# Kernel tuning notes

Measured on AMD Instinct MI355X. Metric: run time of the kernel, lower is better.

## Reference

```python
import jax, jax.numpy as jnp
import numpy as np

N = 50000      # nodes
E = 800000     # edges
IN = 128       # in_channels
HID = 64       # hidden_channels (per head)
HEADS = 2      # GAT heads
OUT = 64       # out_channels (classes)


def segment_softmax(e, seg, num_segments):
    # softmax of per-edge scores grouped by destination node
    m = jax.ops.segment_max(e, seg, num_segments=num_segments)
    ex = jnp.exp(e - m[seg])
    s = jax.ops.segment_sum(ex, seg, num_segments=num_segments)
    return ex / s[seg]


def setup_inputs() -> dict:
    key = jax.random.key(0)
    ks = jax.random.split(key, 12)
    sc = 0.05
    return {
        "x": jax.random.normal(ks[0], (N, IN), dtype=jnp.float32),
        "edge_index": jax.random.randint(ks[1], (2, E), 0, N),
        # GATConv params: lin (no bias), att_src/att_dst, output bias
        "W1": jax.random.normal(ks[2], (IN, HEADS * HID), dtype=jnp.float32) * sc,
        "att_src": jax.random.normal(ks[3], (HEADS, HID), dtype=jnp.float32) * sc,
        "att_dst": jax.random.normal(ks[4], (HEADS, HID), dtype=jnp.float32) * sc,
        "b1": jnp.zeros((HEADS * HID,), dtype=jnp.float32),
        # TransformerConv params (heads=1): q/k/v linears + skip linear
        "Wq": jax.random.normal(ks[5], (HEADS * HID, OUT), dtype=jnp.float32) * sc,
        "bq": jnp.zeros((OUT,), dtype=jnp.float32),
        "Wk": jax.random.normal(ks[6], (HEADS * HID, OUT), dtype=jnp.float32) * sc,
        "bk": jnp.zeros((OUT,), dtype=jnp.float32),
        "Wv": jax.random.normal(ks[7], (HEADS * HID, OUT), dtype=jnp.float32) * sc,
        "bv": jnp.zeros((OUT,), dtype=jnp.float32),
        "Wskip": jax.random.normal(ks[8], (HEADS * HID, OUT), dtype=jnp.float32) * sc,
        "bskip": jnp.zeros((OUT,), dtype=jnp.float32),
    }


def reference(x, edge_index, W1, att_src, att_dst, b1,
              Wq, bq, Wk, bk, Wv, bv, Wskip, bskip):
    n = x.shape[0]
    # ---- GATConv (concat=True, add_self_loops=True, negative_slope=0.2) ----
    loops = jnp.arange(n)
    src = jnp.concatenate([edge_index[0], loops])  # message source j
    dst = jnp.concatenate([edge_index[1], loops])  # message target i
    h = (x @ W1).reshape(n, HEADS, HID)            # [N,H,C]
    a_src = (h * att_src).sum(-1)                  # [N,H]
    a_dst = (h * att_dst).sum(-1)                  # [N,H]
    e = jax.nn.leaky_relu(a_src[src] + a_dst[dst], 0.2)   # [E+N,H]
    alpha = segment_softmax(e, dst, n)                     # [E+N,H]
    out1 = jax.ops.segment_sum(alpha[..., None] * h[src], dst, num_segments=n)
    x1 = jax.nn.relu(out1.reshape(n, HEADS * HID) + b1)    # [N,H*C]
    # ---- TransformerConv (heads=1, root_weight=True, no self-loops) ----
    q = x1 @ Wq + bq
    k = x1 @ Wk + bk
    v = x1 @ Wv + bv
    s2, d2 = edge_index[0], edge_index[1]
    scores = (q[d2] * k[s2]).sum(-1) / jnp.sqrt(jnp.float32(OUT))  # [E]
    al = segment_softmax(scores, d2, n)
    agg = jax.ops.segment_sum(al[:, None] * v[s2], d2, num_segments=n)
    out = agg + x1 @ Wskip + bskip
    return jax.nn.log_softmax(out, axis=1)
```

## Files before the change

kernel.cpp:

```cpp
#include <hip/hip_runtime.h>
#include <math.h>

typedef unsigned short u16;
typedef unsigned int u32;
typedef unsigned char u8;

using bf16x8 = __attribute__((ext_vector_type(8))) short;
using f32x4  = __attribute__((ext_vector_type(4))) float;
typedef __attribute__((ext_vector_type(2))) float vf2;

#define CAP 4096

__device__ __forceinline__ float lrelu02(float x){ return x > 0.f ? x : 0.2f * x; }

__device__ __forceinline__ float bf2f(u16 u){
  union { u32 i; float f; } v; v.i = ((u32)u) << 16; return v.f;
}
__device__ __forceinline__ u16 f2bf(float f){
  union { float ff; u32 i; } v; v.ff = f;
  u32 x = v.i;
  return (u16)((x + 0x7fffu + ((x >> 16) & 1u)) >> 16);
}
__device__ __forceinline__ u32 pack2(float lo, float hi){
  return (u32)f2bf(lo) | ((u32)f2bf(hi) << 16);
}
__device__ __forceinline__ u8 f2fp8(float v){
  return (u8)(__builtin_amdgcn_cvt_pk_fp8_f32(v, v, 0, false) & 0xff);
}
__device__ __forceinline__ vf2 fma2(vf2 a, vf2 b, vf2 c){
  return __builtin_elementwise_fma(a, b, c);
}

__global__ __launch_bounds__(256) void prep_w_kernel(const float* __restrict__ W1,
                                                     const float* __restrict__ Wq,
                                                     const float* __restrict__ Wk,
                                                     const float* __restrict__ Wv,
                                                     const float* __restrict__ Ws,
                                                     const float* __restrict__ att_src,
                                                     const float* __restrict__ att_dst,
                                                     u16* __restrict__ w1t,
                                                     u16* __restrict__ wt2,
                                                     u16* __restrict__ wxt,
                                                     int* __restrict__ bcur){
  int idx = blockIdx.x * 256 + threadIdx.x;
  if (idx < 16384){
    int j = idx >> 7, k = idx & 127;
    w1t[j * 128 + k] = f2bf(W1[k * 128 + j]);
  } else if (idx < 49152){
    int i = idx - 16384;
    int mat = i >> 13;
    int r = i & 8191;
    int j = r >> 7, k = r & 127;
    const float* W = (mat == 0) ? Wq : (mat == 1) ? Wk : (mat == 2) ? Wv : Ws;
    wt2[(mat * 64 + j) * 128 + k] = f2bf(W[k * 64 + j]);
  } else if (idx < 49664){
    int i = idx - 49152;
    int j = i >> 7, k = i & 127;
    const float* av = (j & 2) ? att_dst : att_src;
    int head = j & 1;
    float s = 0.f;
#pragma unroll 8
    for (int c = 0; c < 64; c++) s += W1[k * 128 + head * 64 + c] * av[head * 64 + c];
    wxt[j * 128 + k] = f2bf(s);
  } else if (idx < 51200){
    int i = idx - 49664;
    wxt[512 + i] = 0;
  } else if (idx < 51712){
    int b = idx - 51200;
    bcur[b] = b * CAP;
  }
}

__global__ __launch_bounds__(256) void gemm1_mfma(const float* __restrict__ x,
                                                  const u16* __restrict__ w1t,
                                                  const u16* __restrict__ wxt,
                                                  u8* __restrict__ h8,
                                                  float* __restrict__ asrc,
                                                  float* __restrict__ adst, int n){
  __shared__ u8 lds8[64 * 128];
  int wid = threadIdx.x >> 6, lane = threadIdx.x & 63;
  int rl = lane & 15, kh = lane >> 4;
  int br = blockIdx.x * 64 + wid * 16;
  int arow = br + rl; if (arow > n - 1) arow = n - 1;
  const float* ab = x + (size_t)arow * 128 + kh * 8;
  f32x4 acc[9];
#pragma unroll
  for (int t = 0; t < 9; t++) acc[t] = (f32x4){0.f, 0.f, 0.f, 0.f};
#pragma unroll
  for (int ks = 0; ks < 4; ks++){
    float4 xa = *(const float4*)(ab + ks * 32);
    float4 xb = *(const float4*)(ab + ks * 32 + 4);
    union { bf16x8 v; u32 w[4]; } au;
    au.w[0] = pack2(xa.x, xa.y);
    au.w[1] = pack2(xa.z, xa.w);
    au.w[2] = pack2(xb.x, xb.y);
    au.w[3] = pack2(xb.z, xb.w);
    bf16x8 a = au.v;
#pragma unroll
    for (int t = 0; t < 8; t++){
      bf16x8 b = *(const bf16x8*)(w1t + (size_t)(t * 16 + rl) * 128 + ks * 32 + kh * 8);
      acc[t] = __builtin_amdgcn_mfma_f32_16x16x32_bf16(a, b, acc[t], 0, 0, 0);
    }
    bf16x8 bx = *(const bf16x8*)(wxt + (size_t)rl * 128 + ks * 32 + kh * 8);
    acc[8] = __builtin_amdgcn_mfma_f32_16x16x32_bf16(a, bx, acc[8], 0, 0, 0);
  }
#pragma unroll
  for (int r = 0; r < 4; r++){
    int rloc = wid * 16 + kh * 4 + r;
#pragma unroll
    for (int t = 0; t < 8; t++)
      lds8[rloc * 128 + t * 16 + rl] = f2fp8(acc[t][r]);
    int orow = br + kh * 4 + r;
    if (orow < n && rl < 4){
      float vlv = acc[8][r];
      if (rl < 2) asrc[orow * 2 + rl] = vlv;
      else        adst[orow * 2 + (rl - 2)] = vlv;
    }
  }
  int rrow = wid * 16 + (lane >> 2);
  int cb = (lane & 3) * 32;
  int grow = blockIdx.x * 64 + rrow;
  if (grow < n){
    uint4 v0 = *(const uint4*)&lds8[rrow * 128 + cb];
    uint4 v1 = *(const uint4*)&lds8[rrow * 128 + cb + 16];
    uint4* gp = (uint4*)(h8 + (size_t)grow * 128 + cb);
    gp[0] = v0;
    gp[1] = v1;
  }
}

__global__ __launch_bounds__(256) void gemm2_mfma(const u16* __restrict__ x1bf,
                                                  const u16* __restrict__ wt2,
                                                  const float* __restrict__ bq,
                                                  const float* __restrict__ bk,
                                                  const float* __restrict__ bv,
                                                  const float* __restrict__ bs,
                                                  float* __restrict__ q,
                                                  u8* __restrict__ kv8,
                                                  float* __restrict__ skip, int n){
  int wid = threadIdx.x >> 6, lane = threadIdx.x & 63;
  int rl = lane & 15, kh = lane >> 4;
  int br = blockIdx.x * 64 + wid * 16;
  int arow = br + rl; if (arow > n - 1) arow = n - 1;
  const u16* abase = x1bf + (size_t)arow * 128 + kh * 8;
  f32x4 acc[16];
#pragma unroll
  for (int t = 0; t < 16; t++) acc[t] = (f32x4){0.f, 0.f, 0.f, 0.f};
#pragma unroll
  for (int ks = 0; ks < 4; ks++){
    bf16x8 a = *(const bf16x8*)(abase + ks * 32);
#pragma unroll
    for (int t = 0; t < 16; t++){
      bf16x8 b = *(const bf16x8*)(wt2 + (size_t)(t * 16 + rl) * 128 + ks * 32 + kh * 8);
      acc[t] = __builtin_amdgcn_mfma_f32_16x16x32_bf16(a, b, acc[t], 0, 0, 0);
    }
  }
  float bias_t[16];
#pragma unroll
  for (int t = 0; t < 16; t++){
    const float* bb = (t < 4) ? bq : (t < 8) ? bk : (t < 12) ? bv : bs;
    bias_t[t] = bb[(t & 3) * 16 + rl];
  }
  int orow0 = br + kh * 4;
#pragma unroll
  for (int r = 0; r < 4; r++){
    int orow = orow0 + r;
    if (orow >= n) continue;
#pragma unroll
    for (int t = 0; t < 16; t++){
      int c = (t & 3) * 16 + rl;
      float val = acc[t][r] + bias_t[t];
      if (t < 4)       q[(size_t)orow * 64 + c]    = val;
      else if (t < 8)  kv8[(size_t)orow * 128 + (c >> 3) * 16 + (c & 7)]     = f2fp8(val);
      else if (t < 12) kv8[(size_t)orow * 128 + (c >> 3) * 16 + 8 + (c & 7)] = f2fp8(val);
      else             skip[(size_t)orow * 64 + c] = val;
    }
  }
}

__global__ __launch_bounds__(256) void multisplit_kernel(const int* __restrict__ src,
                                                         const int* __restrict__ dst,
                                                         int* __restrict__ bcur,
                                                         uint2* __restrict__ ebuf, int E){
  __shared__ int h[512];
  __shared__ int gb[512];
  __shared__ int cur[512];
  int tid = threadIdx.x;
  for (int i = tid; i < 512; i += 256){ h[i] = 0; cur[i] = 0; }
  __syncthreads();
  int base = blockIdx.x * 4096;
  int myd[16];
#pragma unroll
  for (int i = 0; i < 16; i++){
    int e = base + i * 256 + tid;
    myd[i] = (e < E) ? dst[e] : -1;
    if (myd[i] >= 0) atomicAdd(&h[myd[i] >> 7], 1);
  }
  __syncthreads();
  for (int i = tid; i < 512; i += 256){
    int c = h[i];
    gb[i] = c ? atomicAdd(&bcur[i], c) : 0;
  }
  __syncthreads();
#pragma unroll
  for (int i = 0; i < 16; i++){
    if (myd[i] >= 0){
      int e = base + i * 256 + tid;
      int b = myd[i] >> 7;
      int r = atomicAdd(&cur[b], 1);
      uint2 ed; ed.x = (u32)src[e]; ed.y = (u32)myd[i];
      ebuf[gb[b] + r] = ed;
    }
  }
}

__global__ __launch_bounds__(256) void bucket_csr_kernel(const uint2* __restrict__ ebuf,
                                                         const int* __restrict__ bcur,
                                                         const float* __restrict__ asrc,
                                                         const float* __restrict__ adst,
                                                         uint2* __restrict__ offs,
                                                         uint2* __restrict__ cpe,
                                                         int n){
  __shared__ int deg[128];
  __shared__ int loff[128];
  __shared__ int cur[128];
  int b = blockIdx.x, tid = threadIdx.x;
  int base = b * CAP, end = bcur[b];
  if (tid < 128) deg[tid] = 0;
  __syncthreads();
  for (int e = base + tid; e < end; e += 256)
    atomicAdd(&deg[ebuf[e].y & 127], 1);
  __syncthreads();
  if (tid < 64){
    int v0 = deg[2 * tid], v1 = deg[2 * tid + 1];
    int s = v0 + v1, incl = s;
#pragma unroll
    for (int o = 1; o < 64; o <<= 1){
      int t = __shfl_up(incl, o);
      if (tid >= o) incl += t;
    }
    int excl = incl - s;
    loff[2 * tid] = excl; loff[2 * tid + 1] = excl + v0;
  }
  __syncthreads();
  int node0 = b << 7;
  if (tid < 128){
    cur[tid] = loff[tid];
    int node = node0 + tid;
    if (node < n){
      uint2 ov;
      ov.x = (u32)(base + loff[tid]);
      ov.y = (u32)(base + loff[tid] + deg[tid]);
      offs[node] = ov;
    }
  }
  __syncthreads();
  for (int e = base + tid; e < end; e += 256){
    uint2 ed = ebuf[e];
    int li = (int)(ed.y & 127);
    int r = atomicAdd(&cur[li], 1);
    int sj = (int)ed.x;
    float2 as = ((const float2*)asrc)[sj];
    float2 ad = ((const float2*)adst)[node0 + li];
    uint2 cv;
    cv.x = (u32)sj;
    cv.y = pack2(__expf(lrelu02(as.x + ad.x)),
                 __expf(lrelu02(as.y + ad.y)));
    cpe[base + r] = cv;
  }
}

__global__ __launch_bounds__(256) void gat_agg_kernel(const u8* __restrict__ h8,
                                                      const float* __restrict__ asrc,
                                                      const float* __restrict__ adst,
                                                      const uint2* __restrict__ offs,
                                                      const uint2* __restrict__ cpe,
                                                      const float* __restrict__ b1,
                                                      u16* __restrict__ x1bf, int n){
  int node = blockIdx.x * 4 + (threadIdx.x >> 6);
  int lane = threadIdx.x & 63;
  if (node >= n) return;
  uint2 ov = offs[node];
  int s0 = (int)ov.x;
  int d  = (int)(ov.y - ov.x);
  int g = lane >> 3;
  int sub = lane & 7;
  int chb = sub * 16;
  int head = sub >> 2;
  float2 ad  = ((const float2*)adst)[node];
  float2 asl = ((const float2*)asrc)[node];
  float ad_own = head ? ad.y : ad.x;
  float pself = __expf(lrelu02((head ? asl.y : asl.x) + ad_own));
  vf2 acc[8];
#pragma unroll
  for (int i = 0; i < 8; i++) acc[i] = (vf2){0.f, 0.f};
  float ps = 0.f;
#pragma unroll 2
  for (int base = 0; base < d; base += 8){
    int idx = base + g;
    bool valid = idx < d;
    int ee = s0 + (valid ? idx : d - 1);
    uint2 ce = cpe[ee];
    int sj = (int)ce.x;
    float p = valid ? bf2f((u16)(head ? (ce.y >> 16) : (ce.y & 0xffffu))) : 0.f;
    ps += p;
    uint4 w = *(const uint4*)(h8 + (size_t)sj * 128 + chb);
    vf2 p2 = {p, p};
    acc[0] = fma2(p2, __builtin_amdgcn_cvt_pk_f32_fp8((int)w.x, false), acc[0]);
    acc[1] = fma2(p2, __builtin_amdgcn_cvt_pk_f32_fp8((int)w.x, true),  acc[1]);
    acc[2] = fma2(p2, __builtin_amdgcn_cvt_pk_f32_fp8((int)w.y, false), acc[2]);
    acc[3] = fma2(p2, __builtin_amdgcn_cvt_pk_f32_fp8((int)w.y, true),  acc[3]);
    acc[4] = fma2(p2, __builtin_amdgcn_cvt_pk_f32_fp8((int)w.z, false), acc[4]);
    acc[5] = fma2(p2, __builtin_amdgcn_cvt_pk_f32_fp8((int)w.z, true),  acc[5]);
    acc[6] = fma2(p2, __builtin_amdgcn_cvt_pk_f32_fp8((int)w.w, false), acc[6]);
    acc[7] = fma2(p2, __builtin_amdgcn_cvt_pk_f32_fp8((int)w.w, true),  acc[7]);
  }
#pragma unroll
  for (int o = 8; o <= 32; o <<= 1){
#pragma unroll
    for (int i = 0; i < 8; i++){
      acc[i][0] += __shfl_xor(acc[i][0], o);
      acc[i][1] += __shfl_xor(acc[i][1], o);
    }
    ps += __shfl_xor(ps, o);
  }
  if (lane < 8){
    float st = ps + pself;
    uint4 w = *(const uint4*)(h8 + (size_t)node * 128 + chb);
    vf2 pf2 = {pself, pself};
    acc[0] = fma2(pf2, __builtin_amdgcn_cvt_pk_f32_fp8((int)w.x, false), acc[0]);
    acc[1] = fma2(pf2, __builtin_amdgcn_cvt_pk_f32_fp8((int)w.x, true),  acc[1]);
    acc[2] = fma2(pf2, __builtin_amdgcn_cvt_pk_f32_fp8((int)w.y, false), acc[2]);
    acc[3] = fma2(pf2, __builtin_amdgcn_cvt_pk_f32_fp8((int)w.y, true),  acc[3]);
    acc[4] = fma2(pf2, __builtin_amdgcn_cvt_pk_f32_fp8((int)w.z, false), acc[4]);
    acc[5] = fma2(pf2, __builtin_amdgcn_cvt_pk_f32_fp8((int)w.z, true),  acc[5]);
    acc[6] = fma2(pf2, __builtin_amdgcn_cvt_pk_f32_fp8((int)w.w, false), acc[6]);
    acc[7] = fma2(pf2, __builtin_amdgcn_cvt_pk_f32_fp8((int)w.w, true),  acc[7]);
    const float4* bp = (const float4*)(b1 + chb);
    float4 bv0 = bp[0], bv1 = bp[1], bv2 = bp[2], bv3 = bp[3];
    float bb[16] = {bv0.x, bv0.y, bv0.z, bv0.w, bv1.x, bv1.y, bv1.z, bv1.w,
                    bv2.x, bv2.y, bv2.z, bv2.w, bv3.x, bv3.y, bv3.z, bv3.w};
    float inv = 1.f / st;
    u32 wv[8];
#pragma unroll
    for (int i = 0; i < 8; i++){
      float v0 = fmaxf(acc[i][0] * inv + bb[2*i],   0.f);
      float v1 = fmaxf(acc[i][1] * inv + bb[2*i+1], 0.f);
      wv[i] = pack2(v0, v1);
    }
    uint4 o0 = {wv[0], wv[1], wv[2], wv[3]};
    uint4 o1 = {wv[4], wv[5], wv[6], wv[7]};
    u16* xp = x1bf + (size_t)node * 128 + chb;
    *(uint4*)xp = o0;
    *(uint4*)(xp + 8) = o1;
  }
}

__global__ __launch_bounds__(256) void trans_agg_kernel(const float* __restrict__ q,
                                                        const u8* __restrict__ kv8,
                                                        const float* __restrict__ skip,
                                                        const uint2* __restrict__ offs,
                                                        const uint2* __restrict__ cpe,
                                                        float* __restrict__ out, int n){
  int node = blockIdx.x * 4 + (threadIdx.x >> 6);
  int lane = threadIdx.x & 63;
  if (node >= n) return;
  uint2 ov = offs[node];
  int s0 = (int)ov.x;
  int d  = (int)(ov.y - ov.x);
  int g = lane >> 3;
  int sub = lane & 7;
  const vf2* qp = (const vf2*)(q + (size_t)node * 64 + sub * 8);
  vf2 q0 = qp[0], q1 = qp[1], q2 = qp[2], q3 = qp[3];
  vf2 acc[4];
#pragma unroll
  for (int i = 0; i < 4; i++) acc[i] = (vf2){0.f, 0.f};
  float ps = 0.f;
#pragma unroll 2
  for (int base = 0; base < d; base += 8){
    int idx = base + g;
    bool valid = idx < d;
    int sj = (int)cpe[s0 + (valid ? idx : d - 1)].x;
    uint4 w = *(const uint4*)(kv8 + (size_t)sj * 128 + sub * 16);
    vf2 d2 = {0.f, 0.f};
    d2 = fma2(q0, __builtin_amdgcn_cvt_pk_f32_fp8((int)w.x, false), d2);
    d2 = fma2(q1, __builtin_amdgcn_cvt_pk_f32_fp8((int)w.x, true),  d2);
    d2 = fma2(q2, __builtin_amdgcn_cvt_pk_f32_fp8((int)w.y, false), d2);
    d2 = fma2(q3, __builtin_amdgcn_cvt_pk_f32_fp8((int)w.y, true),  d2);
    float part = d2[0] + d2[1];
    part += __shfl_xor(part, 1);
    part += __shfl_xor(part, 2);
    part += __shfl_xor(part, 4);
    float p = valid ? __expf(part * 0.125f) : 0.f;
    ps += p;
    vf2 p2 = {p, p};
    acc[0] = fma2(p2, __builtin_amdgcn_cvt_pk_f32_fp8((int)w.z, false), acc[0]);
    acc[1] = fma2(p2, __builtin_amdgcn_cvt_pk_f32_fp8((int)w.z, true),  acc[1]);
    acc[2] = fma2(p2, __builtin_amdgcn_cvt_pk_f32_fp8((int)w.w, false), acc[2]);
    acc[3] = fma2(p2, __builtin_amdgcn_cvt_pk_f32_fp8((int)w.w, true),  acc[3]);
  }
#pragma unroll
  for (int o = 8; o <= 32; o <<= 1){
#pragma unroll
    for (int i = 0; i < 4; i++){
      acc[i][0] += __shfl_xor(acc[i][0], o);
      acc[i][1] += __shfl_xor(acc[i][1], o);
    }
    ps += __shfl_xor(ps, o);
  }
  if (lane < 8){
    const float4* sp = (const float4*)(skip + (size_t)node * 64 + sub * 8);
    float4 s0v = sp[0], s1v = sp[1];
    float sk[8] = {s0v.x, s0v.y, s0v.z, s0v.w, s1v.x, s1v.y, s1v.z, s1v.w};
    float inv = (d > 0) ? 1.f / ps : 0.f;
    float val[8];
    float mx = -3.0e38f;
#pragma unroll
    for (int i = 0; i < 8; i++){
      val[i] = sk[i] + acc[i >> 1][i & 1] * inv;
      mx = fmaxf(mx, val[i]);
    }
    mx = fmaxf(mx, __shfl_xor(mx, 1));
    mx = fmaxf(mx, __shfl_xor(mx, 2));
    mx = fmaxf(mx, __shfl_xor(mx, 4));
    float se = 0.f;
#pragma unroll
    for (int i = 0; i < 8; i++){ val[i] -= mx; se += __expf(val[i]); }
    se += __shfl_xor(se, 1);
    se += __shfl_xor(se, 2);
    se += __shfl_xor(se, 4);
    float lse = __logf(se);
    float* op = out + (size_t)node * 64 + sub * 8;
    float4 o0 = {val[0] - lse, val[1] - lse, val[2] - lse, val[3] - lse};
    float4 o4 = {val[4] - lse, val[5] - lse, val[6] - lse, val[7] - lse};
    *(float4*)(op)     = o0;
    *(float4*)(op + 4) = o4;
  }
}

extern "C" void kernel_launch(void* const* d_in, const int* in_sizes, int n_in,
                              void* d_out, int out_size, void* d_ws, size_t ws_size,
                              hipStream_t stream) {
  const float* x       = (const float*)d_in[0];
  const int*   ei      = (const int*)d_in[1];
  const float* W1      = (const float*)d_in[2];
  const float* att_src = (const float*)d_in[3];
  const float* att_dst = (const float*)d_in[4];
  const float* b1      = (const float*)d_in[5];
  const float* Wq = (const float*)d_in[6];  const float* bq = (const float*)d_in[7];
  const float* Wk = (const float*)d_in[8];  const float* bk = (const float*)d_in[9];
  const float* Wv = (const float*)d_in[10]; const float* bv = (const float*)d_in[11];
  const float* Ws = (const float*)d_in[12]; const float* bs = (const float*)d_in[13];
  float* out = (float*)d_out;

  int n = in_sizes[0] / 128;
  int E = in_sizes[1] / 2;
  const int* src = ei;
  const int* dst = ei + E;
  int nb = (n + 127) >> 7;

  char* w = (char*)d_ws;
  auto alloc = [&](size_t bytes) -> void* {
    void* p = (void*)w;
    w += (bytes + 255) & ~(size_t)255;
    return p;
  };
  u8*   h8   = (u8*)alloc((size_t)n * 128);
  float* asrc = (float*)alloc((size_t)n * 2 * 4);
  float* adst = (float*)alloc((size_t)n * 2 * 4);
  u16*  x1bf = (u16*)alloc((size_t)n * 128 * 2);
  float* qq   = (float*)alloc((size_t)n * 64 * 4);
  u8*   kv8  = (u8*)alloc((size_t)n * 128);
  float* skip = (float*)alloc((size_t)n * 64 * 4);
  uint2* offs = (uint2*)alloc((size_t)n * 8);
  uint2* ebuf = (uint2*)alloc((size_t)nb * CAP * 8);
  uint2* cpe  = (uint2*)alloc((size_t)nb * CAP * 8);
  int* bcur   = (int*)alloc(516 * 4);
  u16*  w1t  = (u16*)alloc((size_t)128 * 128 * 2);
  u16*  wt2  = (u16*)alloc((size_t)256 * 128 * 2);
  u16*  wxt  = (u16*)alloc((size_t)16 * 128 * 2);

  int eblocks = (E + 4095) / 4096;

  prep_w_kernel<<<203, 256, 0, stream>>>(W1, Wq, Wk, Wv, Ws, att_src, att_dst,
                                         w1t, wt2, wxt, bcur);
  gemm1_mfma<<<(n + 63) / 64, 256, 0, stream>>>(x, w1t, wxt, h8, asrc, adst, n);

  multisplit_kernel<<<eblocks, 256, 0, stream>>>(src, dst, bcur, ebuf, E);
  bucket_csr_kernel<<<nb, 256, 0, stream>>>(ebuf, bcur, asrc, adst, offs, cpe, n);

  gat_agg_kernel<<<(n + 3) / 4, 256, 0, stream>>>(h8, asrc, adst, offs, cpe,
                                                  b1, x1bf, n);

  gemm2_mfma<<<(n + 63) / 64, 256, 0, stream>>>(x1bf, wt2, bq, bk, bv, bs,
                                                qq, kv8, skip, n);
  trans_agg_kernel<<<(n + 3) / 4, 256, 0, stream>>>(qq, kv8, skip, offs, cpe,
                                                    out, n);
}
```

Baseline: 161.6 us.

## Split GEMM output columns across waves to raise block count in both GEMMs

```diff
diff --git a/kernel.cpp b/kernel.cpp
--- a/kernel.cpp
+++ b/kernel.cpp
@@ -77,15 +77,16 @@
                                                   u8* __restrict__ h8,
                                                   float* __restrict__ asrc,
                                                   float* __restrict__ adst, int n){
-  __shared__ u8 lds8[64 * 128];
+  __shared__ u8 lds8[32 * 128];
   int wid = threadIdx.x >> 6, lane = threadIdx.x & 63;
+  int rowgrp = wid >> 1, half = wid & 1;
   int rl = lane & 15, kh = lane >> 4;
-  int br = blockIdx.x * 64 + wid * 16;
+  int br = blockIdx.x * 32 + rowgrp * 16;
   int arow = br + rl; if (arow > n - 1) arow = n - 1;
   const float* ab = x + (size_t)arow * 128 + kh * 8;
-  f32x4 acc[9];
-#pragma unroll
-  for (int t = 0; t < 9; t++) acc[t] = (f32x4){0.f, 0.f, 0.f, 0.f};
+  f32x4 acc[5];
+#pragma unroll
+  for (int t = 0; t < 5; t++) acc[t] = (f32x4){0.f, 0.f, 0.f, 0.f};
 #pragma unroll
   for (int ks = 0; ks < 4; ks++){
     float4 xa = *(const float4*)(ab + ks * 32);
@@ -97,35 +98,37 @@
     au.w[3] = pack2(xb.z, xb.w);
     bf16x8 a = au.v;
 #pragma unroll
-    for (int t = 0; t < 8; t++){
-      bf16x8 b = *(const bf16x8*)(w1t + (size_t)(t * 16 + rl) * 128 + ks * 32 + kh * 8);
+    for (int t = 0; t < 4; t++){
+      bf16x8 b = *(const bf16x8*)(w1t + (size_t)((half * 4 + t) * 16 + rl) * 128 + ks * 32 + kh * 8);
       acc[t] = __builtin_amdgcn_mfma_f32_16x16x32_bf16(a, b, acc[t], 0, 0, 0);
     }
-    bf16x8 bx = *(const bf16x8*)(wxt + (size_t)rl * 128 + ks * 32 + kh * 8);
-    acc[8] = __builtin_amdgcn_mfma_f32_16x16x32_bf16(a, bx, acc[8], 0, 0, 0);
+    if (half == 0){
+      bf16x8 bx = *(const bf16x8*)(wxt + (size_t)rl * 128 + ks * 32 + kh * 8);
+      acc[4] = __builtin_amdgcn_mfma_f32_16x16x32_bf16(a, bx, acc[4], 0, 0, 0);
+    }
   }
 #pragma unroll
   for (int r = 0; r < 4; r++){
-    int rloc = wid * 16 + kh * 4 + r;
-#pragma unroll
-    for (int t = 0; t < 8; t++)
-      lds8[rloc * 128 + t * 16 + rl] = f2fp8(acc[t][r]);
-    int orow = br + kh * 4 + r;
-    if (orow < n && rl < 4){
-      float vlv = acc[8][r];
-      if (rl < 2) asrc[orow * 2 + rl] = vlv;
-      else        adst[orow * 2 + (rl - 2)] = vlv;
-    }
-  }
-  int rrow = wid * 16 + (lane >> 2);
-  int cb = (lane & 3) * 32;
-  int grow = blockIdx.x * 64 + rrow;
+    int rloc = rowgrp * 16 + kh * 4 + r;
+#pragma unroll
+    for (int t = 0; t < 4; t++)
+      lds8[rloc * 128 + half * 64 + t * 16 + rl] = f2fp8(acc[t][r]);
+    if (half == 0){
+      int orow = br + kh * 4 + r;
+      if (orow < n && rl < 4){
+        float vlv = acc[4][r];
+        if (rl < 2) asrc[orow * 2 + rl] = vlv;
+        else        adst[orow * 2 + (rl - 2)] = vlv;
+      }
+    }
+  }
+  __syncthreads();
+  int row = threadIdx.x >> 3;
+  int cb = (threadIdx.x & 7) * 16;
+  int grow = blockIdx.x * 32 + row;
   if (grow < n){
-    uint4 v0 = *(const uint4*)&lds8[rrow * 128 + cb];
-    uint4 v1 = *(const uint4*)&lds8[rrow * 128 + cb + 16];
-    uint4* gp = (uint4*)(h8 + (size_t)grow * 128 + cb);
-    gp[0] = v0;
-    gp[1] = v1;
+    uint4 v0 = *(const uint4*)&lds8[row * 128 + cb];
+    *(uint4*)(h8 + (size_t)grow * 128 + cb) = v0;
   }
 }
 
@@ -140,40 +143,38 @@
                                                   float* __restrict__ skip, int n){
   int wid = threadIdx.x >> 6, lane = threadIdx.x & 63;
   int rl = lane & 15, kh = lane >> 4;
-  int br = blockIdx.x * 64 + wid * 16;
+  int br = blockIdx.x * 16;
   int arow = br + rl; if (arow > n - 1) arow = n - 1;
   const u16* abase = x1bf + (size_t)arow * 128 + kh * 8;
-  f32x4 acc[16];
-#pragma unroll
-  for (int t = 0; t < 16; t++) acc[t] = (f32x4){0.f, 0.f, 0.f, 0.f};
+  f32x4 acc[4];
+#pragma unroll
+  for (int t = 0; t < 4; t++) acc[t] = (f32x4){0.f, 0.f, 0.f, 0.f};
 #pragma unroll
   for (int ks = 0; ks < 4; ks++){
     bf16x8 a = *(const bf16x8*)(abase + ks * 32);
 #pragma unroll
-    for (int t = 0; t < 16; t++){
-      bf16x8 b = *(const bf16x8*)(wt2 + (size_t)(t * 16 + rl) * 128 + ks * 32 + kh * 8);
+    for (int t = 0; t < 4; t++){
+      bf16x8 b = *(const bf16x8*)(wt2 + (size_t)(wid * 64 + t * 16 + rl) * 128 + ks * 32 + kh * 8);
       acc[t] = __builtin_amdgcn_mfma_f32_16x16x32_bf16(a, b, acc[t], 0, 0, 0);
     }
   }
-  float bias_t[16];
-#pragma unroll
-  for (int t = 0; t < 16; t++){
-    const float* bb = (t < 4) ? bq : (t < 8) ? bk : (t < 12) ? bv : bs;
-    bias_t[t] = bb[(t & 3) * 16 + rl];
-  }
+  const float* bb = (wid == 0) ? bq : (wid == 1) ? bk : (wid == 2) ? bv : bs;
+  float bias_t[4];
+#pragma unroll
+  for (int t = 0; t < 4; t++) bias_t[t] = bb[t * 16 + rl];
   int orow0 = br + kh * 4;
 #pragma unroll
   for (int r = 0; r < 4; r++){
     int orow = orow0 + r;
     if (orow >= n) continue;
 #pragma unroll
-    for (int t = 0; t < 16; t++){
-      int c = (t & 3) * 16 + rl;
+    for (int t = 0; t < 4; t++){
+      int c = t * 16 + rl;
       float val = acc[t][r] + bias_t[t];
-      if (t < 4)       q[(size_t)orow * 64 + c]    = val;
-      else if (t < 8)  kv8[(size_t)orow * 128 + (c >> 3) * 16 + (c & 7)]     = f2fp8(val);
-      else if (t < 12) kv8[(size_t)orow * 128 + (c >> 3) * 16 + 8 + (c & 7)] = f2fp8(val);
-      else             skip[(size_t)orow * 64 + c] = val;
+      if (wid == 0)      q[(size_t)orow * 64 + c]    = val;
+      else if (wid == 1) kv8[(size_t)orow * 128 + (c >> 3) * 16 + (c & 7)]     = f2fp8(val);
+      else if (wid == 2) kv8[(size_t)orow * 128 + (c >> 3) * 16 + 8 + (c & 7)] = f2fp8(val);
+      else               skip[(size_t)orow * 64 + c] = val;
     }
   }
 }
@@ -484,7 +485,7 @@
 
   prep_w_kernel<<<203, 256, 0, stream>>>(W1, Wq, Wk, Wv, Ws, att_src, att_dst,
                                          w1t, wt2, wxt, bcur);
-  gemm1_mfma<<<(n + 63) / 64, 256, 0, stream>>>(x, w1t, wxt, h8, asrc, adst, n);
+  gemm1_mfma<<<(n + 31) / 32, 256, 0, stream>>>(x, w1t, wxt, h8, asrc, adst, n);
 
   multisplit_kernel<<<eblocks, 256, 0, stream>>>(src, dst, bcur, ebuf, E);
   bucket_csr_kernel<<<nb, 256, 0, stream>>>(ebuf, bcur, asrc, adst, offs, cpe, n);
@@ -492,7 +493,7 @@
   gat_agg_kernel<<<(n + 3) / 4, 256, 0, stream>>>(h8, asrc, adst, offs, cpe,
                                                   b1, x1bf, n);
 
-  gemm2_mfma<<<(n + 63) / 64, 256, 0, stream>>>(x1bf, wt2, bq, bk, bv, bs,
+  gemm2_mfma<<<(n + 15) / 16, 256, 0, stream>>>(x1bf, wt2, bq, bk, bv, bs,
                                                 qq, kv8, skip, n);
   trans_agg_kernel<<<(n + 3) / 4, 256, 0, stream>>>(qq, kv8, skip, offs, cpe,
                                                     out, n);
```

Measured after the change: 161.0 us. No clear change (-0.4%).
